# Kernel tuning notes

Measured on AMD Instinct MI355X. Metric: run time of the kernel, lower is better.

## Reference

```python
import jax, jax.numpy as jnp
import numpy as np

N = 50000   # total nodes (50 graphs x 1000 nodes)
E = 500000  # total edges (avg degree 10)
G = 50      # number of graphs in the batch
IN = 128    # in_dim
H = 4       # attn_head
HID = [64, 128]  # graph_hiddens
SLOPE = 0.2      # negative_slope


def setup_inputs() -> dict:
    key = jax.random.key(0)
    ks = jax.random.split(key, 12)
    nodes_per_g = N // G
    edges_per_g = E // G
    # edges stay inside their own graph block (batched-graph structure)
    off = (jnp.arange(E) // edges_per_g) * nodes_per_g
    edge_src = (jax.random.randint(ks[0], (E,), 0, nodes_per_g) + off).astype(jnp.int32)
    edge_dst = (jax.random.randint(ks[1], (E,), 0, nodes_per_g) + off).astype(jnp.int32)
    node_graph = (jnp.arange(N) // nodes_per_g).astype(jnp.int32)

    def lin(k, i, o):
        return (jax.random.normal(k, (i, o), jnp.float32) / np.sqrt(i)).astype(jnp.float32)

    return dict(
        x=jax.random.normal(ks[2], (N, IN), jnp.float32),
        edge_src=edge_src, edge_dst=edge_dst, node_graph=node_graph,
        Wl1=lin(ks[3], IN, H * HID[0]), bl1=jnp.zeros((H * HID[0],), jnp.float32),
        Wr1=lin(ks[4], IN, H * HID[0]), br1=jnp.zeros((H * HID[0],), jnp.float32),
        attn1=jax.random.normal(ks[5], (H, HID[0]), jnp.float32) * 0.1,
        Wl2=lin(ks[6], HID[0], H * HID[1]), bl2=jnp.zeros((H * HID[1],), jnp.float32),
        Wr2=lin(ks[7], HID[0], H * HID[1]), br2=jnp.zeros((H * HID[1],), jnp.float32),
        attn2=jax.random.normal(ks[8], (H, HID[1]), jnp.float32) * 0.1,
        gate_w=lin(ks[9], HID[1], 1), gate_b=jnp.zeros((1,), jnp.float32),
    )


def _gat_layer(x, src, dst, Wl, bl, Wr, br, attn, n_heads, d_out):
    """DGL GATv2Conv (share_weights=False, no dropout) + maxpool over heads."""
    n = x.shape[0]
    fs = (x @ Wl + bl).reshape(n, n_heads, d_out)  # fc_src -> [N,H,D]
    fd = (x @ Wr + br).reshape(n, n_heads, d_out)  # fc_dst -> [N,H,D]
    # per-edge GATv2 logits: attn . leaky_relu(fs_u + fd_v)
    e = jax.nn.leaky_relu(fs[src] + fd[dst], SLOPE)      # [E,H,D]
    logits = jnp.einsum('ehd,hd->eh', e, attn)           # [E,H]
    # edge softmax over incoming edges of each destination node
    m = jax.ops.segment_max(logits, dst, num_segments=n)  # [N,H]
    a = jnp.exp(logits - m[dst])
    s = jax.ops.segment_sum(a, dst, num_segments=n)
    alpha = a / s[dst]                                   # [E,H]
    out = jax.ops.segment_sum(alpha[:, :, None] * fs[src], dst, num_segments=n)  # [N,H,D]
    # MaxPool1d(attn_head) over the head dimension -> [N,D]
    return out.max(axis=1)


def reference(x, edge_src, edge_dst, node_graph,
              Wl1, bl1, Wr1, br1, attn1,
              Wl2, bl2, Wr2, br2, attn2,
              gate_w, gate_b):
    h = _gat_layer(x, edge_src, edge_dst, Wl1, bl1, Wr1, br1, attn1, H, HID[0])
    h = _gat_layer(h, edge_src, edge_dst, Wl2, bl2, Wr2, br2, attn2, H, HID[1])
    # GlobalAttentionPooling: softmax(gate_nn(h)) per graph, weighted sum
    gate = (h @ gate_w + gate_b)[:, 0]                      # [N]
    gm = jax.ops.segment_max(gate, node_graph, num_segments=G)
    ga = jnp.exp(gate - gm[node_graph])
    gs = jax.ops.segment_sum(ga, node_graph, num_segments=G)
    alpha = (ga / gs[node_graph])[:, None]                  # [N,1]
    return jax.ops.segment_sum(alpha * h, node_graph, num_segments=G)  # [G, HID[1]]
```

## Files before the change

kernel.cpp:

```cpp
#include <hip/hip_runtime.h>
#include <hip/hip_bf16.h>


#define NN 50000
#define EE 500000
#define GG 50
#define NPG 1000
#define HH 4
#define NB_E ((EE + 255) / 256)
#define NB_W 512

typedef unsigned short ushort_t;
typedef unsigned int uint_t;
typedef __attribute__((ext_vector_type(8))) short bf16x8;
typedef __attribute__((ext_vector_type(4))) float f32x4;
typedef __attribute__((ext_vector_type(2))) float f32x2;

__device__ __forceinline__ ushort_t bf16r(float f) {
  __hip_bfloat16 h = __float2bfloat16(f);
  return *reinterpret_cast<ushort_t*>(&h);
}

__device__ __forceinline__ f32x2 up2v(uint_t u) {
  f32x2 r;
  r.x = __uint_as_float(u << 16);
  r.y = __uint_as_float(u & 0xffff0000u);
  return r;
}


__global__ void prep_count(const int* __restrict__ dst, int* __restrict__ counts,
                           const float* __restrict__ Wl1, const float* __restrict__ Wr1,
                           const float* __restrict__ Wl2, const float* __restrict__ Wr2,
                           ushort_t* __restrict__ BW1, ushort_t* __restrict__ BW2) {
  const int b = blockIdx.x;
  if (b < NB_E) {
    int i = b * 256 + threadIdx.x;
    if (i < EE) atomicAdd(&counts[dst[i]], 1);
  } else {
    int i = (b - NB_E) * 256 + threadIdx.x;
    if (i < 512 * 128) {
      int n = i >> 7, k = i & 127;
      const float* W = (n < 256) ? Wl1 : Wr1;
      BW1[i] = bf16r(W[(size_t)k * 256 + (n & 255)]);
    } else {
      int j = i - 512 * 128;
      int n = j >> 6, k = j & 63;
      const float* W = (n < 512) ? Wl2 : Wr2;
      BW2[j] = bf16r(W[(size_t)k * 512 + (n & 511)]);
    }
  }
}


__global__ void scan_block(const int* __restrict__ in, int* __restrict__ out,
                           int* __restrict__ bsum, int n) {
  __shared__ int tmp[256];
  int t = threadIdx.x;
  int i = blockIdx.x * 256 + t;
  int v = (i < n) ? in[i] : 0;
  tmp[t] = v;
  __syncthreads();
  for (int off = 1; off < 256; off <<= 1) {
    int a = (t >= off) ? tmp[t - off] : 0;
    __syncthreads();
    tmp[t] += a;
    __syncthreads();
  }
  if (i < n) out[i] = tmp[t] - v;
  if (t == 255) bsum[blockIdx.x] = tmp[t];
}

__global__ void scan_bsum(int* __restrict__ bsum, int nb) {
  __shared__ int tmp[256];
  int t = threadIdx.x;
  int v = (t < nb) ? bsum[t] : 0;
  tmp[t] = v;
  __syncthreads();
  for (int off = 1; off < 256; off <<= 1) {
    int a = (t >= off) ? tmp[t - off] : 0;
    __syncthreads();
    tmp[t] += a;
    __syncthreads();
  }
  if (t < nb) bsum[t] = tmp[t] - v;
}

__global__ void scan_add(int* __restrict__ out, const int* __restrict__ bsum,
                         int* __restrict__ cursor, int n) {
  int i = blockIdx.x * 256 + threadIdx.x;
  if (i < n) {
    out[i] += bsum[blockIdx.x];
    cursor[i] = 0;
  }
}

__global__ void scatter_edges(const int* __restrict__ src, const int* __restrict__ dst,
                              const int* __restrict__ rowstart, int* __restrict__ cursor,
                              int* __restrict__ csr_src) {
  int i = blockIdx.x * 256 + threadIdx.x;
  if (i < EE) {
    int d = dst[i];
    int p = atomicAdd(&cursor[d], 1);
    csr_src[rowstart[d] + p] = src[i];
  }
}


template<int KDIM, bool AF32>
__global__ __launch_bounds__(256)
void gemm_mfma(const float* __restrict__ Af, const ushort_t* __restrict__ Ab,
               const ushort_t* __restrict__ BW,
               const float* __restrict__ bl, const float* __restrict__ br, int nhalf,
               ushort_t* __restrict__ C, int nstride) {
  constexpr int RS = 72;
  __shared__ __align__(16) ushort_t As[128 * RS];
  __shared__ __align__(16) ushort_t Bs[128 * RS];
  const int t = threadIdx.x;
  const int m0 = blockIdx.x * 128, n0 = blockIdx.y * 128;
  const int lane = t & 63, wv = t >> 6;
  const int l16 = lane & 15, quad = lane >> 4;

  f32x4 acc[2][8];
#pragma unroll
  for (int b = 0; b < 2; ++b)
#pragma unroll
    for (int n = 0; n < 8; ++n) acc[b][n] = (f32x4){0.f, 0.f, 0.f, 0.f};

  for (int k0 = 0; k0 < KDIM; k0 += 64) {
    __syncthreads();
    if (AF32) {
      const int r = t >> 4, c4 = t & 15;
#pragma unroll
      for (int p = 0; p < 8; ++p) {
        int m = m0 + r + p * 16;
        int ms = (m < NN) ? m : NN - 1;
        float4 v = *(const float4*)(Af + (size_t)ms * KDIM + k0 + c4 * 4);
        uint2 pk;
        pk.x = (uint_t)bf16r(v.x) | ((uint_t)bf16r(v.y) << 16);
        pk.y = (uint_t)bf16r(v.z) | ((uint_t)bf16r(v.w) << 16);
        *(uint2*)(As + (r + p * 16) * RS + c4 * 4) = pk;
      }
    } else {
      const int r = t >> 3, seg = t & 7;
#pragma unroll
      for (int p = 0; p < 4; ++p) {
        int m = m0 + r + p * 32;
        int ms = (m < NN) ? m : NN - 1;
        *(uint4*)(As + (r + p * 32) * RS + seg * 8) =
            *(const uint4*)(Ab + (size_t)ms * KDIM + k0 + seg * 8);
      }
    }
    {
      const int r = t >> 3, seg = t & 7;
#pragma unroll
      for (int p = 0; p < 4; ++p) {
        *(uint4*)(Bs + (r + p * 32) * RS + seg * 8) =
            *(const uint4*)(BW + (size_t)(n0 + r + p * 32) * KDIM + k0 + seg * 8);
      }
    }
    __syncthreads();
#pragma unroll
    for (int kk = 0; kk < 2; ++kk) {
      bf16x8 a[2];
#pragma unroll
      for (int b = 0; b < 2; ++b)
        a[b] = *(const bf16x8*)(As + (wv * 32 + b * 16 + l16) * RS + kk * 32 + quad * 8);
#pragma unroll
      for (int n = 0; n < 8; ++n) {
        bf16x8 bb = *(const bf16x8*)(Bs + (n * 16 + l16) * RS + kk * 32 + quad * 8);
        acc[0][n] = __builtin_amdgcn_mfma_f32_16x16x32_bf16(a[0], bb, acc[0][n], 0, 0, 0);
        acc[1][n] = __builtin_amdgcn_mfma_f32_16x16x32_bf16(a[1], bb, acc[1][n], 0, 0, 0);
      }
    }
  }
  const float* bp = (n0 < nhalf) ? bl : br;
  const int nb = (n0 < nhalf) ? n0 : n0 - nhalf;
#pragma unroll
  for (int n = 0; n < 8; ++n) {
    const int col = n0 + n * 16 + l16;
    const float bv = bp[nb + n * 16 + l16];
#pragma unroll
    for (int b = 0; b < 2; ++b) {
      const int rowb = m0 + wv * 32 + b * 16 + quad * 4;
#pragma unroll
      for (int r = 0; r < 4; ++r) {
        if (rowb + r < NN)
          C[(size_t)(rowb + r) * nstride + col] = bf16r(acc[b][n][r] + bv);
      }
    }
  }
}


template<int N32> struct UV;
template<> struct UV<2> { typedef uint2 T; };
template<> struct UV<4> { typedef uint4 T; };

#define GAT_SLOTS ((NN / 4 + 7) / 8)
#define GAT_GRID  (GAT_SLOTS * 8)

template<int D, int STRIDE, bool OUTBF, bool GATE>
__global__ __launch_bounds__(256)
void gat_layer(const ushort_t* __restrict__ fsb, const ushort_t* __restrict__ fdb,
               const float* __restrict__ attn,
               const int* __restrict__ rowstart, const int* __restrict__ deg,
               const int* __restrict__ csr_src,
               float4* __restrict__ out4, ushort_t* __restrict__ outb,
               const float* __restrict__ gw, float* __restrict__ gate) {
  constexpr int DPL = D / 16;
  constexpr int NU  = DPL / 2;
  constexpr int NV4 = DPL / 4;
  constexpr int D4  = D / 4;
  typedef typename UV<NU>::T LT;

  const int b    = blockIdx.x;
  const int slot = (b & 7) * GAT_SLOTS + (b >> 3);
  if (slot >= NN / 4) return;
  const int lane = threadIdx.x & 63;
  const int wvid = threadIdx.x >> 6;
  const int v    = (slot << 2) + wvid;
  const int h    = lane >> 4;
  const int g16  = lane & 15;
  const int foff = h * D + g16 * DPL;

  f32x2 at2[NU], fd2[NU];
  {
    const float* ap = attn + foff;
#pragma unroll
    for (int j = 0; j < NU; ++j) { at2[j].x = ap[2 * j]; at2[j].y = ap[2 * j + 1]; }
    LT raw = *reinterpret_cast<const LT*>(fdb + (size_t)v * STRIDE + foff);
    const uint_t* rw = reinterpret_cast<const uint_t*>(&raw);
#pragma unroll
    for (int j = 0; j < NU; ++j) fd2[j] = up2v(rw[j]);
  }
  const int start = __builtin_amdgcn_readfirstlane(rowstart[v]);
  const int n     = __builtin_amdgcn_readfirstlane(deg[v]);
  const int* cp   = csr_src + start;

  float s = 0.f;
  f32x2 acc2[NU];
#pragma unroll
  for (int j = 0; j < NU; ++j) acc2[j] = (f32x2){0.f, 0.f};

  if (n > 0) {
    LT r0 = *reinterpret_cast<const LT*>(fsb + (size_t)cp[0] * STRIDE + foff);
    LT r1 = r0;
    if (n > 1)
      r1 = *reinterpret_cast<const LT*>(fsb + (size_t)cp[1] * STRIDE + foff);
    for (int e = 0; e < n; ++e) {
      const LT cur = r0;
      r0 = r1;
      if (e + 2 < n)
        r1 = *reinterpret_cast<const LT*>(fsb + (size_t)cp[e + 2] * STRIDE + foff);
      const uint_t* rw = reinterpret_cast<const uint_t*>(&cur);
      f32x2 f0[NU];
#pragma unroll
      for (int j = 0; j < NU; ++j) f0[j] = up2v(rw[j]);
      f32x2 p2 = (f32x2){0.f, 0.f};
#pragma unroll
      for (int j = 0; j < NU; ++j) {
        f32x2 t = f0[j] + fd2[j];
        f32x2 l = __builtin_elementwise_max(t, t * 0.2f);
        p2 = __builtin_elementwise_fma(l, at2[j], p2);
      }
      float p = p2.x + p2.y;
      p += __shfl_xor(p, 1);
      p += __shfl_xor(p, 2);
      p += __shfl_xor(p, 4);
      p += __shfl_xor(p, 8);
      const float w = __expf(p);
      s += w;
      const f32x2 wv2 = {w, w};
#pragma unroll
      for (int j = 0; j < NU; ++j)
        acc2[j] = __builtin_elementwise_fma(wv2, f0[j], acc2[j]);
    }
  }

  const float rs = (n > 0) ? (1.0f / s) : 0.f;
  float acc[DPL];
#pragma unroll
  for (int j = 0; j < NU; ++j) {
    acc[2 * j]     = acc2[j].x * rs;
    acc[2 * j + 1] = acc2[j].y * rs;
  }
#pragma unroll
  for (int i = 0; i < DPL; ++i) {
    acc[i] = fmaxf(acc[i], __shfl_xor(acc[i], 16));
    acc[i] = fmaxf(acc[i], __shfl_xor(acc[i], 32));
  }
  if constexpr (GATE) {
    const float* gp = gw + g16 * DPL;
    float g = 0.f;
#pragma unroll
    for (int i = 0; i < DPL; ++i) g = fmaf(acc[i], gp[i], g);
    g += __shfl_xor(g, 1);  g += __shfl_xor(g, 2);  g += __shfl_xor(g, 4);
    g += __shfl_xor(g, 8);  g += __shfl_xor(g, 16); g += __shfl_xor(g, 32);
    if (lane == 0) gate[v] = g * 0.25f;
  }
  if (h == 0) {
    if constexpr (OUTBF) {
      ushort4 o;
      o.x = bf16r(acc[0]); o.y = bf16r(acc[1]); o.z = bf16r(acc[2]); o.w = bf16r(acc[3]);
      *reinterpret_cast<ushort4*>(outb + (size_t)v * D + g16 * 4) = o;
    } else {
#pragma unroll
      for (int i = 0; i < NV4; ++i)
        out4[(size_t)v * D4 + g16 * NV4 + i] =
            make_float4(acc[4 * i], acc[4 * i + 1], acc[4 * i + 2], acc[4 * i + 3]);
    }
  }
}


__global__ __launch_bounds__(1024)
void pool_fused(const float* __restrict__ gate, const float* __restrict__ h2,
                float* __restrict__ out) {
  const int g = blockIdx.x, t = threadIdx.x;
  const int lane = t & 63, w = t >> 6;
  __shared__ float a_s[NPG];
  __shared__ float red[16];
  __shared__ float fin;
  __shared__ float part[8][128];

  float gv = (t < NPG) ? gate[g * NPG + t] : -__builtin_inff();
  float m = gv;
  m = fmaxf(m, __shfl_xor(m, 1));  m = fmaxf(m, __shfl_xor(m, 2));
  m = fmaxf(m, __shfl_xor(m, 4));  m = fmaxf(m, __shfl_xor(m, 8));
  m = fmaxf(m, __shfl_xor(m, 16)); m = fmaxf(m, __shfl_xor(m, 32));
  if (lane == 0) red[w] = m;
  __syncthreads();
  if (t == 0) {
    float r = red[0];
#pragma unroll
    for (int j = 1; j < 16; ++j) r = fmaxf(r, red[j]);
    fin = r;
  }
  __syncthreads();
  const float gm = fin;

  float ex = (t < NPG) ? __expf(gv - gm) : 0.f;
  float s = ex;
  s += __shfl_xor(s, 1);  s += __shfl_xor(s, 2);  s += __shfl_xor(s, 4);
  s += __shfl_xor(s, 8);  s += __shfl_xor(s, 16); s += __shfl_xor(s, 32);
  if (lane == 0) red[w] = s;
  __syncthreads();
  if (t == 0) {
    float r = 0.f;
#pragma unroll
    for (int j = 0; j < 16; ++j) r += red[j];
    fin = 1.0f / r;
  }
  __syncthreads();
  if (t < NPG) a_s[t] = ex * fin;
  __syncthreads();

  const int d = t & 127;
  const int c = t >> 7;
  float acc = 0.f;
  for (int i = c; i < NPG; i += 8)
    acc = fmaf(a_s[i], h2[(size_t)(g * NPG + i) * 128 + d], acc);
  part[c][d] = acc;
  __syncthreads();
  if (c == 0) {
    float r = acc;
#pragma unroll
    for (int j = 1; j < 8; ++j) r += part[j][d];
    out[g * 128 + d] = r;
  }
}


extern "C" void kernel_launch(void* const* d_in, const int* in_sizes, int n_in,
                              void* d_out, int out_size, void* d_ws, size_t ws_size,
                              hipStream_t stream) {
  const float* x        = (const float*)d_in[0];
  const int*   edge_src = (const int*)d_in[1];
  const int*   edge_dst = (const int*)d_in[2];
  const float* Wl1   = (const float*)d_in[4];
  const float* bl1   = (const float*)d_in[5];
  const float* Wr1   = (const float*)d_in[6];
  const float* br1   = (const float*)d_in[7];
  const float* attn1 = (const float*)d_in[8];
  const float* Wl2   = (const float*)d_in[9];
  const float* bl2   = (const float*)d_in[10];
  const float* Wr2   = (const float*)d_in[11];
  const float* br2   = (const float*)d_in[12];
  const float* attn2 = (const float*)d_in[13];
  const float* gate_w = (const float*)d_in[14];
  float* out = (float*)d_out;

  ushort_t* fsd1 = (ushort_t*)d_ws;
  ushort_t* fsd2 = fsd1;
  ushort_t* h1b  = fsd2 + (size_t)NN * 1024;
  float* h2      = (float*)(h1b + (size_t)NN * 64);
  float* gate    = h2 + (size_t)NN * 128;
  ushort_t* BW1  = (ushort_t*)(gate + NN);
  ushort_t* BW2  = BW1 + 512 * 128;
  int* counts   = (int*)(BW2 + 1024 * 64);
  int* rowstart = counts + NN;
  int* cursor   = rowstart + NN;
  int* csr_src  = cursor + NN;
  int* bsum     = csr_src + EE;

  hipMemsetAsync(counts, 0, NN * sizeof(int), stream);

  const int nbN = (NN + 255) / 256;
  const int nbE = NB_E;
  const int MB  = (NN + 127) / 128;

  prep_count<<<NB_E + NB_W, 256, 0, stream>>>(
      edge_dst, counts, Wl1, Wr1, Wl2, Wr2, BW1, BW2);
  scan_block<<<nbN, 256, 0, stream>>>(counts, rowstart, bsum, NN);
  scan_bsum<<<1, 256, 0, stream>>>(bsum, nbN);
  scan_add<<<nbN, 256, 0, stream>>>(rowstart, bsum, cursor, NN);
  scatter_edges<<<nbE, 256, 0, stream>>>(edge_src, edge_dst, rowstart, cursor, csr_src);

  gemm_mfma<128, true><<<dim3(MB, 4), 256, 0, stream>>>(
      x, nullptr, BW1, bl1, br1, 256, fsd1, 512);
  gat_layer<64, 512, true, false><<<GAT_GRID, 256, 0, stream>>>(
      fsd1, fsd1 + 256, attn1, rowstart, counts, csr_src,
      nullptr, h1b, nullptr, nullptr);
  gemm_mfma<64, false><<<dim3(MB, 8), 256, 0, stream>>>(
      nullptr, h1b, BW2, bl2, br2, 512, fsd2, 1024);
  gat_layer<128, 1024, false, true><<<GAT_GRID, 256, 0, stream>>>(
      fsd2, fsd2 + 512, attn2, rowstart, counts, csr_src,
      (float4*)h2, nullptr, gate_w, gate);

  pool_fused<<<GG, 1024, 0, stream>>>(gate, h2, out);
}
```

Measured before the change: 370.1 us.

## Load GEMM MFMA operands directly from global memory and use exp2 in GAT softmax

The MFMA GEMM no longer stages A and B tiles through shared memory with barriers. Each lane now loads its bf16x8 fragments straight from global memory, converting fp32 to bf16 in registers, and the K loop is fully unrolled. This removes LDS traffic and synchronisation, but makes more uncoalesced global loads and relies on cache hits for B reuse across waves. In the GAT kernel, the attention vector is prescaled by log2(e) so the edge weight can use exp2f instead of __expf.

Result: slower. 414.1 us (+11.9%).

```diff
diff --git a/kernel.cpp b/kernel.cpp
--- a/kernel.cpp
+++ b/kernel.cpp
@@ -113,13 +113,22 @@
                const ushort_t* __restrict__ BW,
                const float* __restrict__ bl, const float* __restrict__ br, int nhalf,
                ushort_t* __restrict__ C, int nstride) {
-  constexpr int RS = 72;
-  __shared__ __align__(16) ushort_t As[128 * RS];
-  __shared__ __align__(16) ushort_t Bs[128 * RS];
   const int t = threadIdx.x;
-  const int m0 = blockIdx.x * 128, n0 = blockIdx.y * 128;
   const int lane = t & 63, wv = t >> 6;
   const int l16 = lane & 15, quad = lane >> 4;
+  const int n0 = blockIdx.y * 128;
+
+  int mrow[2];
+  const ushort_t* arow_b[2];
+  const float* arow_f[2];
+#pragma unroll
+  for (int b = 0; b < 2; ++b) {
+    int m = blockIdx.x * 128 + wv * 32 + b * 16 + l16;
+    mrow[b] = m;
+    int ms = (m < NN) ? m : NN - 1;
+    if (AF32) arow_f[b] = Af + (size_t)ms * KDIM;
+    else      arow_b[b] = Ab + (size_t)ms * KDIM;
+  }
 
   f32x4 acc[2][8];
 #pragma unroll
@@ -127,53 +136,33 @@
 #pragma unroll
     for (int n = 0; n < 8; ++n) acc[b][n] = (f32x4){0.f, 0.f, 0.f, 0.f};
 
-  for (int k0 = 0; k0 < KDIM; k0 += 64) {
-    __syncthreads();
-    if (AF32) {
-      const int r = t >> 4, c4 = t & 15;
-#pragma unroll
-      for (int p = 0; p < 8; ++p) {
-        int m = m0 + r + p * 16;
-        int ms = (m < NN) ? m : NN - 1;
-        float4 v = *(const float4*)(Af + (size_t)ms * KDIM + k0 + c4 * 4);
-        uint2 pk;
-        pk.x = (uint_t)bf16r(v.x) | ((uint_t)bf16r(v.y) << 16);
-        pk.y = (uint_t)bf16r(v.z) | ((uint_t)bf16r(v.w) << 16);
-        *(uint2*)(As + (r + p * 16) * RS + c4 * 4) = pk;
+#pragma unroll
+  for (int k0 = 0; k0 < KDIM; k0 += 32) {
+    bf16x8 a[2];
+#pragma unroll
+    for (int b = 0; b < 2; ++b) {
+      if (AF32) {
+        const float* ap = arow_f[b] + k0 + quad * 8;
+        float4 v0 = *(const float4*)(ap);
+        float4 v1 = *(const float4*)(ap + 4);
+        uint4 pk;
+        pk.x = (uint_t)bf16r(v0.x) | ((uint_t)bf16r(v0.y) << 16);
+        pk.y = (uint_t)bf16r(v0.z) | ((uint_t)bf16r(v0.w) << 16);
+        pk.z = (uint_t)bf16r(v1.x) | ((uint_t)bf16r(v1.y) << 16);
+        pk.w = (uint_t)bf16r(v1.z) | ((uint_t)bf16r(v1.w) << 16);
+        a[b] = *reinterpret_cast<bf16x8*>(&pk);
+      } else {
+        a[b] = *(const bf16x8*)(arow_b[b] + k0 + quad * 8);
       }
-    } else {
-      const int r = t >> 3, seg = t & 7;
-#pragma unroll
-      for (int p = 0; p < 4; ++p) {
-        int m = m0 + r + p * 32;
-        int ms = (m < NN) ? m : NN - 1;
-        *(uint4*)(As + (r + p * 32) * RS + seg * 8) =
-            *(const uint4*)(Ab + (size_t)ms * KDIM + k0 + seg * 8);
-      }
-    }
-    {
-      const int r = t >> 3, seg = t & 7;
-#pragma unroll
-      for (int p = 0; p < 4; ++p) {
-        *(uint4*)(Bs + (r + p * 32) * RS + seg * 8) =
-            *(const uint4*)(BW + (size_t)(n0 + r + p * 32) * KDIM + k0 + seg * 8);
-      }
-    }
-    __syncthreads();
-#pragma unroll
-    for (int kk = 0; kk < 2; ++kk) {
-      bf16x8 a[2];
-#pragma unroll
-      for (int b = 0; b < 2; ++b)
-        a[b] = *(const bf16x8*)(As + (wv * 32 + b * 16 + l16) * RS + kk * 32 + quad * 8);
-#pragma unroll
-      for (int n = 0; n < 8; ++n) {
-        bf16x8 bb = *(const bf16x8*)(Bs + (n * 16 + l16) * RS + kk * 32 + quad * 8);
-        acc[0][n] = __builtin_amdgcn_mfma_f32_16x16x32_bf16(a[0], bb, acc[0][n], 0, 0, 0);
-        acc[1][n] = __builtin_amdgcn_mfma_f32_16x16x32_bf16(a[1], bb, acc[1][n], 0, 0, 0);
-      }
-    }
-  }
+    }
+#pragma unroll
+    for (int n = 0; n < 8; ++n) {
+      bf16x8 bb = *(const bf16x8*)(BW + (size_t)(n0 + n * 16 + l16) * KDIM + k0 + quad * 8);
+      acc[0][n] = __builtin_amdgcn_mfma_f32_16x16x32_bf16(a[0], bb, acc[0][n], 0, 0, 0);
+      acc[1][n] = __builtin_amdgcn_mfma_f32_16x16x32_bf16(a[1], bb, acc[1][n], 0, 0, 0);
+    }
+  }
+
   const float* bp = (n0 < nhalf) ? bl : br;
   const int nb = (n0 < nhalf) ? n0 : n0 - nhalf;
 #pragma unroll
@@ -182,7 +171,7 @@
     const float bv = bp[nb + n * 16 + l16];
 #pragma unroll
     for (int b = 0; b < 2; ++b) {
-      const int rowb = m0 + wv * 32 + b * 16 + quad * 4;
+      const int rowb = blockIdx.x * 128 + wv * 32 + b * 16 + quad * 4;
 #pragma unroll
       for (int r = 0; r < 4; ++r) {
         if (rowb + r < NN)
@@ -228,7 +217,10 @@
   {
     const float* ap = attn + foff;
 #pragma unroll
-    for (int j = 0; j < NU; ++j) { at2[j].x = ap[2 * j]; at2[j].y = ap[2 * j + 1]; }
+    for (int j = 0; j < NU; ++j) {
+      at2[j].x = ap[2 * j] * 1.44269504f;
+      at2[j].y = ap[2 * j + 1] * 1.44269504f;
+    }
     LT raw = *reinterpret_cast<const LT*>(fdb + (size_t)v * STRIDE + foff);
     const uint_t* rw = reinterpret_cast<const uint_t*>(&raw);
 #pragma unroll
@@ -269,7 +261,7 @@
       p += __shfl_xor(p, 2);
       p += __shfl_xor(p, 4);
       p += __shfl_xor(p, 8);
-      const float w = __expf(p);
+      const float w = exp2f(p);
       s += w;
       const f32x2 wv2 = {w, w};
 #pragma unroll
```
